# Optimization experiments

Measured on AMD Instinct MI355X. Metric: run time of the kernel, lower is better.

Reference implementation:

```python
import jax, jax.numpy as jnp
import numpy as np

N, C, OUT, S, NS = 8192, 256, 256, 8, 16  # points, in_planes, out_planes, share_planes, nsample
MID = OUT  # mid_planes = out_planes // 1
H = OUT // S  # linear_w bottleneck width
EPS = 1e-5


def _bn(x, g, b, m, v):
    # inference-mode BatchNorm1d over last (channel) dim
    return (x - m) * jax.lax.rsqrt(v + EPS) * g + b


def _knn_idx(p, k):
    # squared euclidean distances, (N,N); indices of k nearest (self included)
    sq = jnp.sum(p * p, axis=1)
    d = sq[:, None] + sq[None, :] - 2.0 * (p @ p.T)
    return jax.lax.top_k(-jax.lax.stop_gradient(d), k)[1]  # (N, k) int32


def setup_inputs() -> dict:
    key = jax.random.key(0)
    ks = jax.random.split(key, 24)
    g = lambda i, shape, s=0.05: jax.random.normal(ks[i], shape, jnp.float32) * s
    u = lambda i, shape: jax.random.uniform(ks[i], shape, dtype=jnp.float32)
    return {
        'p': u(0, (N, 3)),
        'x': g(1, (N, C), 1.0),
        'w_q': g(2, (C, MID)), 'b_q': jnp.zeros((MID,), jnp.float32),
        'w_k': g(3, (C, MID)), 'b_k': jnp.zeros((MID,), jnp.float32),
        'w_v': g(4, (C, OUT)), 'b_v': jnp.zeros((OUT,), jnp.float32),
        'p_w1': g(5, (3, 3), 0.5), 'p_b1': jnp.zeros((3,), jnp.float32),
        'p_bn_g': u(6, (3,)) + 0.5, 'p_bn_b': g(7, (3,), 0.1),
        'p_bn_m': g(8, (3,), 0.1), 'p_bn_v': u(9, (3,)) + 0.5,
        'p_w2': g(10, (3, OUT), 0.5), 'p_b2': jnp.zeros((OUT,), jnp.float32),
        'w_bn1_g': u(11, (MID,)) + 0.5, 'w_bn1_b': g(12, (MID,), 0.1),
        'w_bn1_m': g(13, (MID,), 0.1), 'w_bn1_v': u(14, (MID,)) + 0.5,
        'w_l1_w': g(15, (MID, H)), 'w_l1_b': jnp.zeros((H,), jnp.float32),
        'w_bn2_g': u(16, (H,)) + 0.5, 'w_bn2_b': g(17, (H,), 0.1),
        'w_bn2_m': g(18, (H,), 0.1), 'w_bn2_v': u(19, (H,)) + 0.5,
        'w_l2_w': g(20, (H, H)), 'w_l2_b': jnp.zeros((H,), jnp.float32),
    }


def reference(p, x, w_q, b_q, w_k, b_k, w_v, b_v,
              p_w1, p_b1, p_bn_g, p_bn_b, p_bn_m, p_bn_v, p_w2, p_b2,
              w_bn1_g, w_bn1_b, w_bn1_m, w_bn1_v, w_l1_w, w_l1_b,
              w_bn2_g, w_bn2_b, w_bn2_m, w_bn2_v, w_l2_w, w_l2_b):
    # PointTransformerLayer forward (single point cloud, o = [N])
    xq = x @ w_q + b_q            # (N, MID)
    xk = x @ w_k + b_k            # (N, MID)
    xv = x @ w_v + b_v            # (N, OUT)

    idx = _knn_idx(p, NS)         # (N, NS) KNN neighbor indices
    pr_xyz = p[idx] - p[:, None, :]   # (N, NS, 3) relative coords (with_xyz=True)
    xk_g = xk[idx]                # (N, NS, MID) gathered keys
    xv_g = xv[idx]                # (N, NS, OUT) gathered values

    # linear_p: Linear(3,3) -> BN -> ReLU -> Linear(3, OUT)
    pr = jax.nn.relu(_bn(pr_xyz @ p_w1 + p_b1, p_bn_g, p_bn_b, p_bn_m, p_bn_v))
    pr = pr @ p_w2 + p_b2         # (N, NS, OUT)

    # einops reduce 'n ns (i j)->n ns j' with j=MID is identity since MID==OUT
    r_qk = xk_g - xq[:, None, :] + pr   # (N, NS, MID)

    # linear_w: BN -> ReLU -> Linear(MID,H) -> BN -> ReLU -> Linear(H,H)
    w = jax.nn.relu(_bn(r_qk, w_bn1_g, w_bn1_b, w_bn1_m, w_bn1_v)) @ w_l1_w + w_l1_b
    w = jax.nn.relu(_bn(w, w_bn2_g, w_bn2_b, w_bn2_m, w_bn2_v)) @ w_l2_w + w_l2_b
    w = jax.nn.softmax(w, axis=1)       # softmax over neighbors (dim=1)

    v = (xv_g + pr).reshape(N, NS, S, H)      # 'n ns (s i) -> n ns s i'
    out = jnp.einsum('ntsi,nti->nsi', v, w)   # weighted aggregation over neighbors
    return out.reshape(N, OUT)
```

## Files before the change

### kernel.cpp

```cpp
#include <hip/hip_runtime.h>
#include <hip/hip_bf16.h>
#include <math.h>

#define N_PTS 8192
#define C_IN  256
#define OUT_C 256
#define NSAMP 16
#define H_W   32
#define EPSBN 1e-5f
#define GDIM  8
#define NCELL (GDIM * GDIM * GDIM)
#define CAPC  768
#define CAP_H 96
#define GEMM_BLKS 384

typedef short bf16x8 __attribute__((ext_vector_type(8)));
typedef float f32x4  __attribute__((ext_vector_type(4)));

__device__ __forceinline__ float dist2(const float4 a, const float4 b) {
  float dot = a.x * b.x + a.y * b.y + a.z * b.z;
  return a.w + b.w - 2.0f * dot;
}

__device__ __forceinline__ unsigned long long make_key(float d, int j) {
  unsigned int di = __float_as_uint(d);
  unsigned int ord = ((int)di >= 0) ? (di ^ 0x80000000u) : ~di;
  return ((unsigned long long)ord << 32) | (unsigned int)j;
}

__device__ __forceinline__ void chain_insert(unsigned long long (&ak)[16], unsigned long long key) {
  if (key < ak[0]) {
    #pragma unroll
    for (int s = 0; s < 15; ++s) {
      unsigned long long mn = ak[s] < key ? ak[s] : key;
      unsigned long long nx = ak[s + 1];
      ak[s] = nx > mn ? nx : mn;
    }
    ak[15] = ak[15] < key ? ak[15] : key;
  }
}

__device__ __forceinline__ float b2f(short s) {
  return __uint_as_float(((unsigned int)(unsigned short)s) << 16);
}
__device__ __forceinline__ short f2b(float v) {
  __hip_bfloat16 h = __float2bfloat16(v);
  short s;
  __builtin_memcpy(&s, &h, 2);
  return s;
}

__global__ __launch_bounds__(256) void prep_kernel(
    const float* __restrict__ p, const float* __restrict__ x,
    const float* __restrict__ wq, const float* __restrict__ wk, const float* __restrict__ wv,
    const float* __restrict__ bq, const float* __restrict__ bk, const float* __restrict__ bv,
    const float* __restrict__ l1w, const float* __restrict__ l2w,
    const float* __restrict__ bn1g, const float* __restrict__ bn1b,
    const float* __restrict__ bn1m, const float* __restrict__ bn1v,
    float4* __restrict__ p4, __hip_bfloat16* __restrict__ Bp, float* __restrict__ biasp,
    __hip_bfloat16* __restrict__ xb,
    __hip_bfloat16* __restrict__ l1wp, __hip_bfloat16* __restrict__ l2wp,
    float* __restrict__ sc1, float* __restrict__ of1,
    int* __restrict__ cursor, int* __restrict__ pt_cell) {
  int tid = blockIdx.x * blockDim.x + threadIdx.x;
  if (tid < 262144) {
    const float* xr = &x[(size_t)tid * 8];
    float4 xa = *(const float4*)xr;
    float4 xc = *(const float4*)(xr + 4);
    bf16x8 v;
    v[0] = f2b(xa.x); v[1] = f2b(xa.y); v[2] = f2b(xa.z); v[3] = f2b(xa.w);
    v[4] = f2b(xc.x); v[5] = f2b(xc.y); v[6] = f2b(xc.z); v[7] = f2b(xc.w);
    *(bf16x8*)&xb[(size_t)tid * 8] = v;
  }
  if (tid < 48 * 32 * 16 * 8) {
    int kj = tid & 7, n = (tid >> 3) & 15, kb = (tid >> 7) & 31, nt = tid >> 12;
    int k = kb * 8 + kj, col = nt * 16 + n;
    float v;
    if (col < 256)      v = wq[k * 256 + col];
    else if (col < 512) v = wk[k * 256 + (col - 256)];
    else                v = wv[k * 256 + (col - 512)];
    Bp[tid] = __float2bfloat16(v);
  }
  if (tid < 768) {
    biasp[tid] = tid < 256 ? bq[tid] : (tid < 512 ? bk[tid - 256] : bv[tid - 512]);
  }
  if (tid < 8192) {
    int kj = tid & 7, n = (tid >> 3) & 15, kb = (tid >> 7) & 31, nt = (tid >> 12) & 1;
    int k = kb * 8 + kj, col = nt * 16 + n;
    l1wp[tid] = __float2bfloat16(l1w[k * 32 + col]);
  }
  if (tid < 1024) {
    int kj = tid & 7, n = (tid >> 3) & 15, kb = (tid >> 7) & 3, nt = (tid >> 9) & 1;
    int k = kb * 8 + kj, col = nt * 16 + n;
    l2wp[tid] = __float2bfloat16(l2w[k * 32 + col]);
  }
  if (tid < 256) {
    float s1 = bn1g[tid] * rsqrtf(bn1v[tid] + EPSBN);
    sc1[tid] = s1;
    of1[tid] = bn1b[tid] - bn1m[tid] * s1;
  }
  if (tid < NCELL) cursor[tid] = 0;
  if (tid < N_PTS) {
    float px = p[tid * 3 + 0], py = p[tid * 3 + 1], pz = p[tid * 3 + 2];
    float sq = px * px;
    sq += py * py;
    sq += pz * pz;
    p4[tid] = make_float4(px, py, pz, sq);
    int cx = min(GDIM - 1, max(0, (int)(px * GDIM)));
    int cy = min(GDIM - 1, max(0, (int)(py * GDIM)));
    int cz = min(GDIM - 1, max(0, (int)(pz * GDIM)));
    pt_cell[tid] = (cz * GDIM + cy) * GDIM + cx;
  }
}

__global__ __launch_bounds__(512) void scatter_scan(
    const float4* __restrict__ p4, const int* __restrict__ pt_cell,
    int* __restrict__ cell_start, int* __restrict__ cursor,
    float4* __restrict__ sp4, int* __restrict__ sidx, int* __restrict__ rank) {
  __shared__ int buf[NCELL];
  const int t = threadIdx.x;
  buf[t] = 0;
  __syncthreads();
  for (int i = t; i < N_PTS; i += 512) atomicAdd(&buf[pt_cell[i]], 1);
  __syncthreads();
  for (int off = 1; off < NCELL; off <<= 1) {
    int add = (t >= off) ? buf[t - off] : 0;
    __syncthreads();
    buf[t] += add;
    __syncthreads();
  }
  if (blockIdx.x == 0) {
    cell_start[t + 1] = buf[t];
    if (t == 0) cell_start[0] = 0;
  }
  const int pid = blockIdx.x * 512 + t;
  const int c = pt_cell[pid];
  const int start = (c == 0) ? 0 : buf[c - 1];
  const int pos = start + atomicAdd(&cursor[c], 1);
  sp4[pos] = p4[pid];
  sidx[pos] = pid;
  rank[pid] = pos;
}

__global__ __launch_bounds__(256) void knn_gemm(
    const float4* __restrict__ sp4, const int* __restrict__ sidx,
    const int* __restrict__ cell_start, int* __restrict__ nbr,
    const __hip_bfloat16* __restrict__ xb, const __hip_bfloat16* __restrict__ Bp,
    const float* __restrict__ biasp, __hip_bfloat16* __restrict__ xqkv) {
  if (blockIdx.x < GEMM_BLKS) {
    const int w = threadIdx.x >> 6;
    const int lane = threadIdx.x & 63;
    const int gw = blockIdx.x * 4 + w;
    const int m0 = (gw & 127) * 64;
    const int nt4 = (gw >> 7) * 4;
    const int n = lane & 15, q = lane >> 4;

    int o[4];
    #pragma unroll
    for (int mi = 0; mi < 4; ++mi) o[mi] = sidx[m0 + mi * 16 + n];

    f32x4 acc[4][4];
    #pragma unroll
    for (int mi = 0; mi < 4; ++mi)
      #pragma unroll
      for (int ni = 0; ni < 4; ++ni) acc[mi][ni] = (f32x4){0.f, 0.f, 0.f, 0.f};

    for (int k0 = 0; k0 < 256; k0 += 32) {
      bf16x8 af[4], bfr[4];
      #pragma unroll
      for (int mi = 0; mi < 4; ++mi)
        af[mi] = *(const bf16x8*)&xb[(size_t)o[mi] * 256 + k0 + q * 8];
      #pragma unroll
      for (int ni = 0; ni < 4; ++ni)
        bfr[ni] = *(const bf16x8*)&Bp[(size_t)(nt4 + ni) * 4096 + (k0 >> 3) * 128 + q * 128 + n * 8];
      #pragma unroll
      for (int mi = 0; mi < 4; ++mi)
        #pragma unroll
        for (int ni = 0; ni < 4; ++ni)
          acc[mi][ni] = __builtin_amdgcn_mfma_f32_16x16x32_bf16(af[mi], bfr[ni], acc[mi][ni], 0, 0, 0);
    }
    #pragma unroll
    for (int ni = 0; ni < 4; ++ni) {
      int col = (nt4 + ni) * 16 + n;
      float b = biasp[col];
      #pragma unroll
      for (int mi = 0; mi < 4; ++mi)
        #pragma unroll
        for (int r = 0; r < 4; ++r)
          xqkv[(size_t)(m0 + mi * 16 + q * 4 + r) * 768 + col] = __float2bfloat16(acc[mi][ni][r] + b);
    }
    return;
  }

  const int kbid = blockIdx.x - GEMM_BLKS;
  const int cell = kbid >> 1;
  const int sub  = kbid & 1;
  const int cs = cell_start[cell], ce = cell_start[cell + 1];
  if (cs + 8 * sub >= ce) return;

  __shared__ float4 cpos[CAPC];
  __shared__ int    cidx[CAPC];
  __shared__ unsigned long long hk_s[8][CAP_H];
  __shared__ unsigned long long okey_s[8][16];
  __shared__ float tv_s[8][64];
  __shared__ int cnt_s[8];
  __shared__ int cell_s0_s[27];
  __shared__ int len_s[27];
  __shared__ int pref_s[28];
  __shared__ int nc_s, total_s;

  const int tid = threadIdx.x;
  const int hcx = cell & 7, hcy = (cell >> 3) & 7, hcz = cell >> 6;

  const int ax0 = max(hcx - 1, 0), ax1 = min(hcx + 1, GDIM - 1);
  const int ay0 = max(hcy - 1, 0), ay1 = min(hcy + 1, GDIM - 1);
  const int az0 = max(hcz - 1, 0), az1 = min(hcz + 1, GDIM - 1);
  const int nx = ax1 - ax0 + 1, ny = ay1 - ay0 + 1, nz = az1 - az0 + 1;
  const int nbc = nx * ny * nz;

  if (tid < nbc) {
    int cx = ax0 + tid % nx;
    int cy = ay0 + (tid / nx) % ny;
    int cz = az0 + tid / (nx * ny);
    int cc = (cz * GDIM + cy) * GDIM + cx;
    int s0 = cell_start[cc];
    cell_s0_s[tid] = s0;
    len_s[tid] = cell_start[cc + 1] - s0;
  }
  __syncthreads();
  if (tid == 0) {
    int off = 0;
    for (int m = 0; m < nbc; ++m) { pref_s[m] = off; off += len_s[m]; }
    pref_s[nbc] = off;
    nc_s = nbc;
    total_s = off;
  }
  __syncthreads();
  const int nc = nc_s, total = total_s;

  {
    const int grp = tid >> 5, ln = tid & 31;
    for (int m = grp; m < nbc; m += 8) {
      int base = pref_s[m], src = cell_s0_s[m];
      int lim = min(len_s[m], CAPC - base);
      for (int i = ln; i < lim; i += 32) {
        cpos[base + i] = sp4[src + i];
        cidx[base + i] = sidx[src + i];
      }
    }
  }
  __syncthreads();

  const int ptl = tid >> 5, slice = tid & 31;

  for (int p0 = cs + 8 * sub; p0 < ce; p0 += 16) {
    const int np = min(8, ce - p0);
    const bool pok = ptl < np;
    const int ld = pok ? (p0 + ptl) : cs;
    const float4 pi = sp4[ld];
    const int orig = sidx[ld];

    if (tid < 8) cnt_s[tid] = 0;
    if (tid < 128) okey_s[tid >> 4][tid & 15] = ~0ULL;
    __syncthreads();

    float t0 = 3.0e38f, t1 = 3.0e38f;
    for (int idx = slice; idx < total; idx += 32) {
      float4 q;
      if (idx < CAPC) q = cpos[idx];
      else {
        int c = 0;
        while (c + 1 < nc && pref_s[c + 1] <= idx) ++c;
        q = sp4[cell_s0_s[c] + (idx - pref_s[c])];
      }
      float d = dist2(pi, q);
      if (d < t1) {
        if (d < t0) { t1 = t0; t0 = d; } else { t1 = d; }
      }
    }
    tv_s[ptl][slice * 2]     = t0;
    tv_s[ptl][slice * 2 + 1] = t1;
    __syncthreads();

    int r0 = 0, r1 = 0;
    #pragma unroll 8
    for (int j = 0; j < 64; ++j) {
      float wv = tv_s[ptl][j];
      r0 += (wv < t0) ? 1 : 0;
      r1 += (wv < t1) ? 1 : 0;
    }
    float cand = fmaxf(r0 <= 15 ? t0 : -3.0e38f, r1 <= 15 ? t1 : -3.0e38f);
    cand = fmaxf(cand, __shfl_xor(cand, 1, 64));
    cand = fmaxf(cand, __shfl_xor(cand, 2, 64));
    cand = fmaxf(cand, __shfl_xor(cand, 4, 64));
    cand = fmaxf(cand, __shfl_xor(cand, 8, 64));
    cand = fmaxf(cand, __shfl_xor(cand, 16, 64));
    const float d16 = cand;

    const float rg = sqrtf(fmaxf(d16, 0.f)) * 1.001f + 1e-4f;
    const int lx = (int)fminf(fmaxf(floorf((pi.x - rg) * GDIM), 0.f), (float)(GDIM - 1));
    const int ux = (int)fminf(fmaxf(floorf((pi.x + rg) * GDIM), 0.f), (float)(GDIM - 1));
    const int ly = (int)fminf(fmaxf(floorf((pi.y - rg) * GDIM), 0.f), (float)(GDIM - 1));
    const int uy = (int)fminf(fmaxf(floorf((pi.y + rg) * GDIM), 0.f), (float)(GDIM - 1));
    const int lz = (int)fminf(fmaxf(floorf((pi.z - rg) * GDIM), 0.f), (float)(GDIM - 1));
    const int uz = (int)fminf(fmaxf(floorf((pi.z + rg) * GDIM), 0.f), (float)(GDIM - 1));
    const bool trigger = (lx < ax0 || ux > ax1 || ly < ay0 || uy > ay1 || lz < az0 || uz > az1);

    if (pok) {
      for (int idx = slice; idx < total; idx += 32) {
        float4 q;
        int qi;
        if (idx < CAPC) { q = cpos[idx]; qi = cidx[idx]; }
        else {
          int c = 0;
          while (c + 1 < nc && pref_s[c + 1] <= idx) ++c;
          int g = cell_s0_s[c] + (idx - pref_s[c]);
          q = sp4[g]; qi = sidx[g];
        }
        float d = dist2(pi, q);
        if (d <= d16) {
          int pos = atomicAdd(&cnt_s[ptl], 1);
          if (pos < CAP_H) hk_s[ptl][pos] = make_key(d, qi);
        }
      }
      if (trigger) {
        for (int cz = lz; cz <= uz; ++cz)
          for (int cy = ly; cy <= uy; ++cy)
            for (int cx = lx; cx <= ux; ++cx) {
              if (cx >= ax0 && cx <= ax1 && cy >= ay0 && cy <= ay1 && cz >= az0 && cz <= az1)
                continue;
              int cc = (cz * GDIM + cy) * GDIM + cx;
              int s0 = cell_start[cc], e0 = cell_start[cc + 1];
              for (int k = s0 + slice; k < e0; k += 32) {
                float d = dist2(pi, sp4[k]);
                if (d <= d16) {
                  int pos = atomicAdd(&cnt_s[ptl], 1);
                  if (pos < CAP_H) hk_s[ptl][pos] = make_key(d, sidx[k]);
                }
              }
            }
      }
    }
    __syncthreads();

    const int cntr = cnt_s[ptl];
    const bool overflow = cntr > CAP_H;
    const int cnt = overflow ? 0 : cntr;

    if (pok) {
      for (int i = slice; i < cnt; i += 32) {
        unsigned long long key = hk_s[ptl][i];
        int rk = 0;
        for (int j = 0; j < cnt; ++j) rk += (hk_s[ptl][j] < key) ? 1 : 0;
        if (rk < 16) okey_s[ptl][rk] = key;
      }
    }
    __syncthreads();

    if (!overflow) {
      if (pok && slice < 16) {
        unsigned long long key = okey_s[ptl][15 - slice];
        nbr[orig * NSAMP + slice] = (int)(key & 0xFFFFFFFFu);
      }
    } else if (pok && slice == 0) {
      unsigned long long akm[16];
      #pragma unroll
      for (int s = 0; s < 16; ++s) akm[s] = ~0ULL;
      for (int idx2 = 0; idx2 < total; ++idx2) {
        float4 q; int qi;
        if (idx2 < CAPC) { q = cpos[idx2]; qi = cidx[idx2]; }
        else {
          int c = 0;
          while (c + 1 < nc && pref_s[c + 1] <= idx2) ++c;
          int g = cell_s0_s[c] + (idx2 - pref_s[c]);
          q = sp4[g]; qi = sidx[g];
        }
        chain_insert(akm, make_key(dist2(pi, q), qi));
      }
      float r;
      if (akm[0] == ~0ULL) r = 1e9f;
      else {
        unsigned int ord = (unsigned int)(akm[0] >> 32);
        unsigned int di = (ord & 0x80000000u) ? (ord ^ 0x80000000u) : ~ord;
        float dd = __uint_as_float(di);
        r = sqrtf(fmaxf(dd, 0.f)) * 1.001f + 1e-4f;
      }
      int flx = (int)fminf(fmaxf(floorf((pi.x - r) * GDIM), 0.f), (float)(GDIM - 1));
      int fux = (int)fminf(fmaxf(floorf((pi.x + r) * GDIM), 0.f), (float)(GDIM - 1));
      int fly = (int)fminf(fmaxf(floorf((pi.y - r) * GDIM), 0.f), (float)(GDIM - 1));
      int fuy = (int)fminf(fmaxf(floorf((pi.y + r) * GDIM), 0.f), (float)(GDIM - 1));
      int flz = (int)fminf(fmaxf(floorf((pi.z - r) * GDIM), 0.f), (float)(GDIM - 1));
      int fuz = (int)fminf(fmaxf(floorf((pi.z + r) * GDIM), 0.f), (float)(GDIM - 1));
      for (int cz = flz; cz <= fuz; ++cz)
        for (int cy = fly; cy <= fuy; ++cy)
          for (int cx = flx; cx <= fux; ++cx) {
            if (cx >= ax0 && cx <= ax1 && cy >= ay0 && cy <= ay1 && cz >= az0 && cz <= az1)
              continue;
            int cc = (cz * GDIM + cy) * GDIM + cx;
            int s0 = cell_start[cc], e0 = cell_start[cc + 1];
            for (int k = s0; k < e0; ++k) {
              float4 q = sp4[k];
              chain_insert(akm, make_key(dist2(pi, q), sidx[k]));
            }
          }
      #pragma unroll
      for (int s = 0; s < 16; ++s) nbr[orig * NSAMP + s] = (int)(akm[s] & 0xFFFFFFFFu);
    }
    __syncthreads();
  }
}

__global__ __launch_bounds__(256) void fused_pt(
    const float4* __restrict__ sp4, const int* __restrict__ sidx, const int* __restrict__ rank,
    const __hip_bfloat16* __restrict__ xqkv, const int* __restrict__ nbr,
    const float* __restrict__ pw1, const float* __restrict__ pb1,
    const float* __restrict__ pbng, const float* __restrict__ pbnb,
    const float* __restrict__ pbnm, const float* __restrict__ pbnv,
    const float* __restrict__ pw2, const float* __restrict__ pb2,
    const float* __restrict__ sc1, const float* __restrict__ of1,
    const __hip_bfloat16* __restrict__ l1wp, const float* __restrict__ l1b,
    const float* __restrict__ bn2g, const float* __restrict__ bn2b,
    const float* __restrict__ bn2m, const float* __restrict__ bn2v,
    const __hip_bfloat16* __restrict__ l2wp, const float* __restrict__ l2b,
    float* __restrict__ out) {
  __shared__ __align__(16) __hip_bfloat16 a_s[2][NSAMP][264];
  __shared__ __align__(16) __hip_bfloat16 h1_s[2][NSAMP][40];
  __shared__ float w_s[2][NSAMP][33];
  __shared__ float q3_s[2][NSAMP][4];
  __shared__ int jn[2][NSAMP];
  __shared__ float psum[2][2][264];
  __shared__ int iorig[2];

  const int b0 = blockIdx.x * 2;
  const int tid = threadIdx.x;

  if (tid < 32) {
    int spt = tid >> 4, t = tid & 15;
    int b = b0 + spt;
    int i = sidx[b];
    if (t == 0) iorig[spt] = i;
    int j = nbr[i * NSAMP + t];
    int k = rank[j];
    jn[spt][t] = k;
    float4 pj = sp4[k];
    float4 pc = sp4[b];
    float rx = pj.x - pc.x;
    float ry = pj.y - pc.y;
    float rz = pj.z - pc.z;
    #pragma unroll
    for (int c3 = 0; c3 < 3; ++c3) {
      float t2 = rx * pw1[0 * 3 + c3] + ry * pw1[1 * 3 + c3] + rz * pw1[2 * 3 + c3] + pb1[c3];
      t2 = (t2 - pbnm[c3]) * rsqrtf(pbnv[c3] + EPSBN) * pbng[c3] + pbnb[c3];
      q3_s[spt][t][c3] = fmaxf(t2, 0.f);
    }
  }
  __syncthreads();

  const int pt = tid >> 7;
  const int t127 = tid & 127;
  const int g = t127 >> 5;
  const int cg = (t127 & 31) * 8;
  const int b = b0 + pt;

  float xqv[8], s1v[8], o1v[8], w20v[8], w21v[8], w22v[8], pb2v[8];
  {
    bf16x8 xq8 = *(const bf16x8*)&xqkv[(size_t)b * 768 + cg];
    #pragma unroll
    for (int u = 0; u < 8; ++u) {
      int c = cg + u;
      xqv[u] = b2f(xq8[u]);
      s1v[u] = sc1[c];
      o1v[u] = of1[c];
      w20v[u] = pw2[c];
      w21v[u] = pw2[256 + c];
      w22v[u] = pw2[512 + c];
      pb2v[u] = pb2[c];
    }
  }

  #pragma unroll
  for (int pass = 0; pass < 4; ++pass) {
    int t = g + pass * 4;
    int k = jn[pt][t];
    float q30 = q3_s[pt][t][0], q31 = q3_s[pt][t][1], q32 = q3_s[pt][t][2];
    bf16x8 xk8 = *(const bf16x8*)&xqkv[(size_t)k * 768 + 256 + cg];
    bf16x8 av;
    #pragma unroll
    for (int u = 0; u < 8; ++u) {
      float prv = q30 * w20v[u] + q31 * w21v[u] + q32 * w22v[u] + pb2v[u];
      float r = b2f(xk8[u]) - xqv[u] + prv;
      av[u] = f2b(fmaxf(r * s1v[u] + o1v[u], 0.f));
    }
    *(bf16x8*)&a_s[pt][t][cg] = av;
  }
  __syncthreads();

  const int w = tid >> 6;
  const int lane = tid & 63;
  const int mpt = w >> 1, hh = w & 1;
  const int nn = lane & 15, q = lane >> 4;
  {
    f32x4 acc = {0.f, 0.f, 0.f, 0.f};
    #pragma unroll
    for (int k0 = 0; k0 < 256; k0 += 32) {
      bf16x8 a = *(const bf16x8*)&a_s[mpt][nn][k0 + q * 8];
      bf16x8 bb = *(const bf16x8*)&l1wp[hh * 4096 + (k0 >> 3) * 128 + q * 128 + nn * 8];
      acc = __builtin_amdgcn_mfma_f32_16x16x32_bf16(a, bb, acc, 0, 0, 0);
    }
    int h = hh * 16 + nn;
    float s2 = bn2g[h] * rsqrtf(bn2v[h] + EPSBN);
    float o2 = bn2b[h] - bn2m[h] * s2;
    float l1bh = l1b[h];
    #pragma unroll
    for (int r = 0; r < 4; ++r)
      h1_s[mpt][q * 4 + r][h] = __float2bfloat16(fmaxf((acc[r] + l1bh) * s2 + o2, 0.f));
  }
  __syncthreads();

  {
    bf16x8 a = *(const bf16x8*)&h1_s[mpt][nn][q * 8];
    bf16x8 bb = *(const bf16x8*)&l2wp[hh * 512 + q * 128 + nn * 8];
    f32x4 z = {0.f, 0.f, 0.f, 0.f};
    f32x4 d = __builtin_amdgcn_mfma_f32_16x16x32_bf16(a, bb, z, 0, 0, 0);
    int h = hh * 16 + nn;
    float l2bh = l2b[h];
    #pragma unroll
    for (int r = 0; r < 4; ++r) w_s[mpt][q * 4 + r][h] = d[r] + l2bh;
  }
  __syncthreads();

  if (tid < 64) {
    int spt = tid >> 5, h = tid & 31;
    float m = -1e30f;
    #pragma unroll
    for (int t = 0; t < NSAMP; ++t) m = fmaxf(m, w_s[spt][t][h]);
    float e[NSAMP];
    float ssum = 0.f;
    #pragma unroll
    for (int t = 0; t < NSAMP; ++t) { e[t] = __expf(w_s[spt][t][h] - m); ssum += e[t]; }
    float inv = 1.f / ssum;
    #pragma unroll
    for (int t = 0; t < NSAMP; ++t) w_s[spt][t][h] = e[t] * inv;
  }
  __syncthreads();

  const int hb = cg & 31;
  float acc8[8];
  #pragma unroll
  for (int u = 0; u < 8; ++u) acc8[u] = 0.f;
  #pragma unroll
  for (int pass = 0; pass < 4; ++pass) {
    int t = g + pass * 4;
    int k = jn[pt][t];
    float q30 = q3_s[pt][t][0], q31 = q3_s[pt][t][1], q32 = q3_s[pt][t][2];
    bf16x8 xv8 = *(const bf16x8*)&xqkv[(size_t)k * 768 + 512 + cg];
    #pragma unroll
    for (int u = 0; u < 8; ++u) {
      float prv = q30 * w20v[u] + q31 * w21v[u] + q32 * w22v[u] + pb2v[u];
      acc8[u] += (b2f(xv8[u]) + prv) * w_s[pt][t][hb + u];
    }
  }
  #pragma unroll
  for (int u = 0; u < 8; ++u) acc8[u] += __shfl_xor(acc8[u], 32, 64);
  if ((lane >> 5) == 0) {
    #pragma unroll
    for (int u = 0; u < 8; ++u) psum[mpt][hh][cg + u] = acc8[u];
  }
  __syncthreads();
  {
    int opt = tid >> 7;
    int c0 = (tid & 127) * 2;
    float v0 = psum[opt][0][c0] + psum[opt][1][c0];
    float v1 = psum[opt][0][c0 + 1] + psum[opt][1][c0 + 1];
    int io = iorig[opt];
    *(float2*)&out[(size_t)io * OUT_C + c0] = make_float2(v0, v1);
  }
}

extern "C" void kernel_launch(void* const* d_in, const int* in_sizes, int n_in,
                              void* d_out, int out_size, void* d_ws, size_t ws_size,
                              hipStream_t stream) {
  const float* p    = (const float*)d_in[0];
  const float* x    = (const float*)d_in[1];
  const float* wq   = (const float*)d_in[2];
  const float* bq   = (const float*)d_in[3];
  const float* wk   = (const float*)d_in[4];
  const float* bk   = (const float*)d_in[5];
  const float* wv   = (const float*)d_in[6];
  const float* bv   = (const float*)d_in[7];
  const float* pw1  = (const float*)d_in[8];
  const float* pb1  = (const float*)d_in[9];
  const float* pbng = (const float*)d_in[10];
  const float* pbnb = (const float*)d_in[11];
  const float* pbnm = (const float*)d_in[12];
  const float* pbnv = (const float*)d_in[13];
  const float* pw2  = (const float*)d_in[14];
  const float* pb2  = (const float*)d_in[15];
  const float* bn1g = (const float*)d_in[16];
  const float* bn1b = (const float*)d_in[17];
  const float* bn1m = (const float*)d_in[18];
  const float* bn1v = (const float*)d_in[19];
  const float* l1w  = (const float*)d_in[20];
  const float* l1b  = (const float*)d_in[21];
  const float* bn2g = (const float*)d_in[22];
  const float* bn2b = (const float*)d_in[23];
  const float* bn2m = (const float*)d_in[24];
  const float* bn2v = (const float*)d_in[25];
  const float* l2w  = (const float*)d_in[26];
  const float* l2b  = (const float*)d_in[27];
  float* out = (float*)d_out;

  char* ws = (char*)d_ws;
  float4* p4       = (float4*)(ws + 0x000000);
  float*  biasp    = (float*)(ws + 0x040000);
  int*    cursor   = (int*)(ws + 0x042800);
  int*    cell_st  = (int*)(ws + 0x043000);
  int*    pt_cell  = (int*)(ws + 0x044000);
  float4* sp4      = (float4*)(ws + 0x050000);
  int*    sidx     = (int*)(ws + 0x070000);
  __hip_bfloat16* l1wp = (__hip_bfloat16*)(ws + 0x080000);
  __hip_bfloat16* l2wp = (__hip_bfloat16*)(ws + 0x084000);
  float*  sc1      = (float*)(ws + 0x085000);
  float*  of1      = (float*)(ws + 0x085800);
  int*    rank     = (int*)(ws + 0x088000);
  int*    nbr      = (int*)(ws + 0x090000);
  __hip_bfloat16* Bp   = (__hip_bfloat16*)(ws + 0x110000);
  __hip_bfloat16* xb   = (__hip_bfloat16*)(ws + 0x170000);
  __hip_bfloat16* xqkv = (__hip_bfloat16*)(ws + 0x570000);

  prep_kernel<<<dim3(1024), dim3(256), 0, stream>>>(
      p, x, wq, wk, wv, bq, bk, bv, l1w, l2w, bn1g, bn1b, bn1m, bn1v,
      p4, Bp, biasp, xb, l1wp, l2wp, sc1, of1, cursor, pt_cell);
  scatter_scan<<<dim3(16), dim3(512), 0, stream>>>(
      p4, pt_cell, cell_st, cursor, sp4, sidx, rank);
  knn_gemm<<<dim3(GEMM_BLKS + NCELL * 2), dim3(256), 0, stream>>>(
      sp4, sidx, cell_st, nbr, xb, Bp, biasp, xqkv);
  fused_pt<<<dim3(N_PTS / 2), dim3(256), 0, stream>>>(
      sp4, sidx, rank, xqkv, nbr, pw1, pb1, pbng, pbnb, pbnm, pbnv, pw2, pb2,
      sc1, of1, l1wp, l1b, bn2g, bn2b, bn2m, bn2v, l2wp, l2b, out);
}
```

Before: 197.9 us.

## Drop LDS cell staging and block barriers in KNN, split cells four ways

The KNN part of knn_gemm no longer stages the 27 neighbour cells into shared memory. It reads sorted positions straight from global memory, one x-contiguous row of cells at a time. All block-wide __syncthreads are removed, so each 32-lane point group works independently and relies on wavefront-level ordering of LDS accesses. Each cell is now split across four blocks instead of two, giving more blocks and less serial work per block. The trade-off is more global and L2 traffic from repeated reads of the same cells, and correctness now depends on implicit in-wave synchronisation.

Result: slower. 212.4 us (+7.3%).

```diff
diff --git a/kernel.cpp b/kernel.cpp
--- a/kernel.cpp
+++ b/kernel.cpp
@@ -10,9 +10,9 @@
 #define EPSBN 1e-5f
 #define GDIM  8
 #define NCELL (GDIM * GDIM * GDIM)
-#define CAPC  768
 #define CAP_H 96
 #define GEMM_BLKS 384
+#define NSUB  4
 
 typedef short bf16x8 __attribute__((ext_vector_type(8)));
 typedef float f32x4  __attribute__((ext_vector_type(4)));
@@ -193,94 +193,48 @@
   }
 
   const int kbid = blockIdx.x - GEMM_BLKS;
-  const int cell = kbid >> 1;
-  const int sub  = kbid & 1;
+  const int cell = kbid >> 2;
+  const int sub  = kbid & 3;
   const int cs = cell_start[cell], ce = cell_start[cell + 1];
   if (cs + 8 * sub >= ce) return;
 
-  __shared__ float4 cpos[CAPC];
-  __shared__ int    cidx[CAPC];
   __shared__ unsigned long long hk_s[8][CAP_H];
   __shared__ unsigned long long okey_s[8][16];
   __shared__ float tv_s[8][64];
   __shared__ int cnt_s[8];
-  __shared__ int cell_s0_s[27];
-  __shared__ int len_s[27];
-  __shared__ int pref_s[28];
-  __shared__ int nc_s, total_s;
 
   const int tid = threadIdx.x;
+  const int ptl = tid >> 5, slice = tid & 31;
   const int hcx = cell & 7, hcy = (cell >> 3) & 7, hcz = cell >> 6;
 
   const int ax0 = max(hcx - 1, 0), ax1 = min(hcx + 1, GDIM - 1);
   const int ay0 = max(hcy - 1, 0), ay1 = min(hcy + 1, GDIM - 1);
   const int az0 = max(hcz - 1, 0), az1 = min(hcz + 1, GDIM - 1);
-  const int nx = ax1 - ax0 + 1, ny = ay1 - ay0 + 1, nz = az1 - az0 + 1;
-  const int nbc = nx * ny * nz;
-
-  if (tid < nbc) {
-    int cx = ax0 + tid % nx;
-    int cy = ay0 + (tid / nx) % ny;
-    int cz = az0 + tid / (nx * ny);
-    int cc = (cz * GDIM + cy) * GDIM + cx;
-    int s0 = cell_start[cc];
-    cell_s0_s[tid] = s0;
-    len_s[tid] = cell_start[cc + 1] - s0;
-  }
-  __syncthreads();
-  if (tid == 0) {
-    int off = 0;
-    for (int m = 0; m < nbc; ++m) { pref_s[m] = off; off += len_s[m]; }
-    pref_s[nbc] = off;
-    nc_s = nbc;
-    total_s = off;
-  }
-  __syncthreads();
-  const int nc = nc_s, total = total_s;
-
-  {
-    const int grp = tid >> 5, ln = tid & 31;
-    for (int m = grp; m < nbc; m += 8) {
-      int base = pref_s[m], src = cell_s0_s[m];
-      int lim = min(len_s[m], CAPC - base);
-      for (int i = ln; i < lim; i += 32) {
-        cpos[base + i] = sp4[src + i];
-        cidx[base + i] = sidx[src + i];
-      }
-    }
-  }
-  __syncthreads();
-
-  const int ptl = tid >> 5, slice = tid & 31;
-
-  for (int p0 = cs + 8 * sub; p0 < ce; p0 += 16) {
-    const int np = min(8, ce - p0);
-    const bool pok = ptl < np;
+
+  for (int p0 = cs + 8 * sub; p0 < ce; p0 += 8 * NSUB) {
+    const bool pok = (p0 + ptl) < ce;
     const int ld = pok ? (p0 + ptl) : cs;
     const float4 pi = sp4[ld];
     const int orig = sidx[ld];
 
-    if (tid < 8) cnt_s[tid] = 0;
-    if (tid < 128) okey_s[tid >> 4][tid & 15] = ~0ULL;
-    __syncthreads();
+    if (slice == 0) cnt_s[ptl] = 0;
+    if (slice < 16) okey_s[ptl][slice] = ~0ULL;
 
     float t0 = 3.0e38f, t1 = 3.0e38f;
-    for (int idx = slice; idx < total; idx += 32) {
-      float4 q;
-      if (idx < CAPC) q = cpos[idx];
-      else {
-        int c = 0;
-        while (c + 1 < nc && pref_s[c + 1] <= idx) ++c;
-        q = sp4[cell_s0_s[c] + (idx - pref_s[c])];
+    for (int cz = az0; cz <= az1; ++cz)
+      for (int cy = ay0; cy <= ay1; ++cy) {
+        int base = (cz * GDIM + cy) * GDIM;
+        int s = cell_start[base + ax0];
+        int e = cell_start[base + ax1 + 1];
+        for (int k = s + slice; k < e; k += 32) {
+          float d = dist2(pi, sp4[k]);
+          if (d < t1) {
+            if (d < t0) { t1 = t0; t0 = d; } else { t1 = d; }
+          }
+        }
       }
-      float d = dist2(pi, q);
-      if (d < t1) {
-        if (d < t0) { t1 = t0; t0 = d; } else { t1 = d; }
-      }
-    }
     tv_s[ptl][slice * 2]     = t0;
     tv_s[ptl][slice * 2 + 1] = t1;
-    __syncthreads();
 
     int r0 = 0, r1 = 0;
     #pragma unroll 8
@@ -307,22 +261,19 @@
     const bool trigger = (lx < ax0 || ux > ax1 || ly < ay0 || uy > ay1 || lz < az0 || uz > az1);
 
     if (pok) {
-      for (int idx = slice; idx < total; idx += 32) {
-        float4 q;
-        int qi;
-        if (idx < CAPC) { q = cpos[idx]; qi = cidx[idx]; }
-        else {
-          int c = 0;
-          while (c + 1 < nc && pref_s[c + 1] <= idx) ++c;
-          int g = cell_s0_s[c] + (idx - pref_s[c]);
-          q = sp4[g]; qi = sidx[g];
+      for (int cz = az0; cz <= az1; ++cz)
+        for (int cy = ay0; cy <= ay1; ++cy) {
+          int base = (cz * GDIM + cy) * GDIM;
+          int s = cell_start[base + ax0];
+          int e = cell_start[base + ax1 + 1];
+          for (int k = s + slice; k < e; k += 32) {
+            float d = dist2(pi, sp4[k]);
+            if (d <= d16) {
+              int pos = atomicAdd(&cnt_s[ptl], 1);
+              if (pos < CAP_H) hk_s[ptl][pos] = make_key(d, sidx[k]);
+            }
+          }
         }
-        float d = dist2(pi, q);
-        if (d <= d16) {
-          int pos = atomicAdd(&cnt_s[ptl], 1);
-          if (pos < CAP_H) hk_s[ptl][pos] = make_key(d, qi);
-        }
-      }
       if (trigger) {
         for (int cz = lz; cz <= uz; ++cz)
           for (int cy = ly; cy <= uy; ++cy)
@@ -341,7 +292,6 @@
             }
       }
     }
-    __syncthreads();
 
     const int cntr = cnt_s[ptl];
     const bool overflow = cntr > CAP_H;
@@ -355,7 +305,6 @@
         if (rk < 16) okey_s[ptl][rk] = key;
       }
     }
-    __syncthreads();
 
     if (!overflow) {
       if (pok && slice < 16) {
@@ -366,17 +315,14 @@
       unsigned long long akm[16];
       #pragma unroll
       for (int s = 0; s < 16; ++s) akm[s] = ~0ULL;
-      for (int idx2 = 0; idx2 < total; ++idx2) {
-        float4 q; int qi;
-        if (idx2 < CAPC) { q = cpos[idx2]; qi = cidx[idx2]; }
-        else {
-          int c = 0;
-          while (c + 1 < nc && pref_s[c + 1] <= idx2) ++c;
-          int g = cell_s0_s[c] + (idx2 - pref_s[c]);
-          q = sp4[g]; qi = sidx[g];
+      for (int cz = az0; cz <= az1; ++cz)
+        for (int cy = ay0; cy <= ay1; ++cy) {
+          int base = (cz * GDIM + cy) * GDIM;
+          int s = cell_start[base + ax0];
+          int e = cell_start[base + ax1 + 1];
+          for (int k = s; k < e; ++k)
+            chain_insert(akm, make_key(dist2(pi, sp4[k]), sidx[k]));
         }
-        chain_insert(akm, make_key(dist2(pi, q), qi));
-      }
       float r;
       if (akm[0] == ~0ULL) r = 1e9f;
       else {
@@ -398,15 +344,12 @@
               continue;
             int cc = (cz * GDIM + cy) * GDIM + cx;
             int s0 = cell_start[cc], e0 = cell_start[cc + 1];
-            for (int k = s0; k < e0; ++k) {
-              float4 q = sp4[k];
-              chain_insert(akm, make_key(dist2(pi, q), sidx[k]));
-            }
+            for (int k = s0; k < e0; ++k)
+              chain_insert(akm, make_key(dist2(pi, sp4[k]), sidx[k]));
           }
       #pragma unroll
       for (int s = 0; s < 16; ++s) nbr[orig * NSAMP + s] = (int)(akm[s] & 0xFFFFFFFFu);
     }
-    __syncthreads();
   }
 }
 
@@ -633,7 +576,7 @@
       p4, Bp, biasp, xb, l1wp, l2wp, sc1, of1, cursor, pt_cell);
   scatter_scan<<<dim3(16), dim3(512), 0, stream>>>(
       p4, pt_cell, cell_st, cursor, sp4, sidx, rank);
-  knn_gemm<<<dim3(GEMM_BLKS + NCELL * 2), dim3(256), 0, stream>>>(
+  knn_gemm<<<dim3(GEMM_BLKS + NCELL * NSUB), dim3(256), 0, stream>>>(
       sp4, sidx, cell_st, nbr, xb, Bp, biasp, xqkv);
   fused_pt<<<dim3(N_PTS / 2), dim3(256), 0, stream>>>(
       sp4, sidx, rank, xqkv, nbr, pw1, pb1, pbng, pbnb, pbnm, pbnv, pw2, pb2,
```

## Split fused KNN+GEMM kernel and store QKV in original point order

Applied to the files above, without the earlier changes.

The QKV GEMM is split out of the combined KNN/GEMM launch into its own kernel, launched before scatter_scan, and now reads x rows in original order instead of through the spatially sorted index. The fused attention kernel switches to original neighbor indices and the original row for q lookups. This removes the sidx indirection from the GEMM and the rank lookup from feature gathers. In exchange it adds a launch and loses the overlap of GEMM blocks with the irregular KNN blocks, and the gathers no longer follow spatial order, which may hurt locality.

Measured after the change: 190.1 us. -4.0%, faster.

```diff
diff --git a/kernel.cpp b/kernel.cpp
--- a/kernel.cpp
+++ b/kernel.cpp
@@ -12,7 +12,6 @@
 #define NCELL (GDIM * GDIM * GDIM)
 #define CAPC  768
 #define CAP_H 96
-#define GEMM_BLKS 384
 
 typedef short bf16x8 __attribute__((ext_vector_type(8)));
 typedef float f32x4  __attribute__((ext_vector_type(4)));
@@ -142,57 +141,52 @@
   rank[pid] = pos;
 }
 
-__global__ __launch_bounds__(256) void knn_gemm(
-    const float4* __restrict__ sp4, const int* __restrict__ sidx,
-    const int* __restrict__ cell_start, int* __restrict__ nbr,
+__global__ __launch_bounds__(256) void gemm_qkv(
     const __hip_bfloat16* __restrict__ xb, const __hip_bfloat16* __restrict__ Bp,
     const float* __restrict__ biasp, __hip_bfloat16* __restrict__ xqkv) {
-  if (blockIdx.x < GEMM_BLKS) {
-    const int w = threadIdx.x >> 6;
-    const int lane = threadIdx.x & 63;
-    const int gw = blockIdx.x * 4 + w;
-    const int m0 = (gw & 127) * 64;
-    const int nt4 = (gw >> 7) * 4;
-    const int n = lane & 15, q = lane >> 4;
-
-    int o[4];
-    #pragma unroll
-    for (int mi = 0; mi < 4; ++mi) o[mi] = sidx[m0 + mi * 16 + n];
-
-    f32x4 acc[4][4];
+  const int w = threadIdx.x >> 6;
+  const int lane = threadIdx.x & 63;
+  const int gw = blockIdx.x * 4 + w;
+  const int m0 = (gw & 127) * 64;
+  const int nt4 = (gw >> 7) * 4;
+  const int n = lane & 15, q = lane >> 4;
+
+  f32x4 acc[4][4];
+  #pragma unroll
+  for (int mi = 0; mi < 4; ++mi)
+    #pragma unroll
+    for (int ni = 0; ni < 4; ++ni) acc[mi][ni] = (f32x4){0.f, 0.f, 0.f, 0.f};
+
+  for (int k0 = 0; k0 < 256; k0 += 32) {
+    bf16x8 af[4], bfr[4];
+    #pragma unroll
+    for (int mi = 0; mi < 4; ++mi)
+      af[mi] = *(const bf16x8*)&xb[(size_t)(m0 + mi * 16 + n) * 256 + k0 + q * 8];
+    #pragma unroll
+    for (int ni = 0; ni < 4; ++ni)
+      bfr[ni] = *(const bf16x8*)&Bp[(size_t)(nt4 + ni) * 4096 + (k0 >> 3) * 128 + q * 128 + n * 8];
     #pragma unroll
     for (int mi = 0; mi < 4; ++mi)
       #pragma unroll
-      for (int ni = 0; ni < 4; ++ni) acc[mi][ni] = (f32x4){0.f, 0.f, 0.f, 0.f};
-
-    for (int k0 = 0; k0 < 256; k0 += 32) {
-      bf16x8 af[4], bfr[4];
+      for (int ni = 0; ni < 4; ++ni)
+        acc[mi][ni] = __builtin_amdgcn_mfma_f32_16x16x32_bf16(af[mi], bfr[ni], acc[mi][ni], 0, 0, 0);
+  }
+  #pragma unroll
+  for (int ni = 0; ni < 4; ++ni) {
+    int col = (nt4 + ni) * 16 + n;
+    float b = biasp[col];
+    #pragma unroll
+    for (int mi = 0; mi < 4; ++mi)
       #pragma unroll
-      for (int mi = 0; mi < 4; ++mi)
-        af[mi] = *(const bf16x8*)&xb[(size_t)o[mi] * 256 + k0 + q * 8];
-      #pragma unroll
-      for (int ni = 0; ni < 4; ++ni)
-        bfr[ni] = *(const bf16x8*)&Bp[(size_t)(nt4 + ni) * 4096 + (k0 >> 3) * 128 + q * 128 + n * 8];
-      #pragma unroll
-      for (int mi = 0; mi < 4; ++mi)
-        #pragma unroll
-        for (int ni = 0; ni < 4; ++ni)
-          acc[mi][ni] = __builtin_amdgcn_mfma_f32_16x16x32_bf16(af[mi], bfr[ni], acc[mi][ni], 0, 0, 0);
-    }
-    #pragma unroll
-    for (int ni = 0; ni < 4; ++ni) {
-      int col = (nt4 + ni) * 16 + n;
-      float b = biasp[col];
-      #pragma unroll
-      for (int mi = 0; mi < 4; ++mi)
-        #pragma unroll
-        for (int r = 0; r < 4; ++r)
-          xqkv[(size_t)(m0 + mi * 16 + q * 4 + r) * 768 + col] = __float2bfloat16(acc[mi][ni][r] + b);
-    }
-    return;
-  }
-
-  const int kbid = blockIdx.x - GEMM_BLKS;
+      for (int r = 0; r < 4; ++r)
+        xqkv[(size_t)(m0 + mi * 16 + q * 4 + r) * 768 + col] = __float2bfloat16(acc[mi][ni][r] + b);
+  }
+}
+
+__global__ __launch_bounds__(256) void knn_grid(
+    const float4* __restrict__ sp4, const int* __restrict__ sidx,
+    const int* __restrict__ cell_start, int* __restrict__ nbr) {
+  const int kbid = blockIdx.x;
   const int cell = kbid >> 1;
   const int sub  = kbid & 1;
   const int cs = cell_start[cell], ce = cell_start[cell + 1];
@@ -398,10 +392,8 @@
               continue;
             int cc = (cz * GDIM + cy) * GDIM + cx;
             int s0 = cell_start[cc], e0 = cell_start[cc + 1];
-            for (int k = s0; k < e0; ++k) {
-              float4 q = sp4[k];
-              chain_insert(akm, make_key(dist2(pi, q), sidx[k]));
-            }
+            for (int k = s0; k < e0; ++k)
+              chain_insert(akm, make_key(dist2(pi, sp4[k]), sidx[k]));
           }
       #pragma unroll
       for (int s = 0; s < 16; ++s) nbr[orig * NSAMP + s] = (int)(akm[s] & 0xFFFFFFFFu);
@@ -427,7 +419,7 @@
   __shared__ __align__(16) __hip_bfloat16 h1_s[2][NSAMP][40];
   __shared__ float w_s[2][NSAMP][33];
   __shared__ float q3_s[2][NSAMP][4];
-  __shared__ int jn[2][NSAMP];
+  __shared__ int jo[2][NSAMP];
   __shared__ float psum[2][2][264];
   __shared__ int iorig[2];
 
@@ -441,7 +433,7 @@
     if (t == 0) iorig[spt] = i;
     int j = nbr[i * NSAMP + t];
     int k = rank[j];
-    jn[spt][t] = k;
+    jo[spt][t] = j;
     float4 pj = sp4[k];
     float4 pc = sp4[b];
     float rx = pj.x - pc.x;
@@ -460,11 +452,11 @@
   const int t127 = tid & 127;
   const int g = t127 >> 5;
   const int cg = (t127 & 31) * 8;
-  const int b = b0 + pt;
+  const int brow = iorig[pt];
 
   float xqv[8], s1v[8], o1v[8], w20v[8], w21v[8], w22v[8], pb2v[8];
   {
-    bf16x8 xq8 = *(const bf16x8*)&xqkv[(size_t)b * 768 + cg];
+    bf16x8 xq8 = *(const bf16x8*)&xqkv[(size_t)brow * 768 + cg];
     #pragma unroll
     for (int u = 0; u < 8; ++u) {
       int c = cg + u;
@@ -481,7 +473,7 @@
   #pragma unroll
   for (int pass = 0; pass < 4; ++pass) {
     int t = g + pass * 4;
-    int k = jn[pt][t];
+    int k = jo[pt][t];
     float q30 = q3_s[pt][t][0], q31 = q3_s[pt][t][1], q32 = q3_s[pt][t][2];
     bf16x8 xk8 = *(const bf16x8*)&xqkv[(size_t)k * 768 + 256 + cg];
     bf16x8 av;
@@ -551,7 +543,7 @@
   #pragma unroll
   for (int pass = 0; pass < 4; ++pass) {
     int t = g + pass * 4;
-    int k = jn[pt][t];
+    int k = jo[pt][t];
     float q30 = q3_s[pt][t][0], q31 = q3_s[pt][t][1], q32 = q3_s[pt][t][2];
     bf16x8 xv8 = *(const bf16x8*)&xqkv[(size_t)k * 768 + 512 + cg];
     #pragma unroll
@@ -631,10 +623,10 @@
   prep_kernel<<<dim3(1024), dim3(256), 0, stream>>>(
       p, x, wq, wk, wv, bq, bk, bv, l1w, l2w, bn1g, bn1b, bn1m, bn1v,
       p4, Bp, biasp, xb, l1wp, l2wp, sc1, of1, cursor, pt_cell);
+  gemm_qkv<<<dim3(384), dim3(256), 0, stream>>>(xb, Bp, biasp, xqkv);
   scatter_scan<<<dim3(16), dim3(512), 0, stream>>>(
       p4, pt_cell, cell_st, cursor, sp4, sidx, rank);
-  knn_gemm<<<dim3(GEMM_BLKS + NCELL * 2), dim3(256), 0, stream>>>(
-      sp4, sidx, cell_st, nbr, xb, Bp, biasp, xqkv);
+  knn_grid<<<dim3(NCELL * 2), dim3(256), 0, stream>>>(sp4, sidx, cell_st, nbr);
   fused_pt<<<dim3(N_PTS / 2), dim3(256), 0, stream>>>(
       sp4, sidx, rank, xqkv, nbr, pw1, pb1, pbng, pbnb, pbnm, pbnv, pw2, pb2,
       sc1, of1, l1wp, l1b, bn2g, bn2b, bn2m, bn2v, l2wp, l2b, out);
```
